# Kernel tuning notes

Measured on AMD Instinct MI355X. Metric: run time of the kernel, lower is better.

Reference implementation:

```python
import jax, jax.numpy as jnp
import numpy as np

N_NODES = 10000
N_EDGES = 160000
IN_C = 32
OUT_C = 32
FC = 32
DIM = 3
RADIUS = 1.0
LN_EPS = 1e-5


def _layernorm(x, g, b):
    mu = jnp.mean(x, axis=-1, keepdims=True)
    var = jnp.mean(jnp.square(x - mu), axis=-1, keepdims=True)
    return (x - mu) * jax.lax.rsqrt(var + LN_EPS) * g + b


def setup_inputs() -> dict:
    key = jax.random.key(0)
    ks = jax.random.split(key, 10)
    inp = {
        "features": jax.random.normal(ks[0], (N_NODES, IN_C), dtype=jnp.float32),
        "hood_coords": jax.random.normal(ks[1], (N_EDGES, DIM), dtype=jnp.float32),
        "source": jax.random.randint(ks[2], (N_EDGES,), 0, N_NODES, dtype=jnp.int32),
        "target": jax.random.randint(ks[3], (N_EDGES,), 0, N_NODES, dtype=jnp.int32),
        # neural field params: Linear(DIM,FC) -> LN -> ReLU -> Linear(FC,FC) -> LN -> ReLU -> Linear(FC, IN_C*OUT_C) -> Tanh
        "W0": jax.random.normal(ks[4], (DIM, FC), dtype=jnp.float32) * 0.3,
        "b0": jnp.zeros((FC,), dtype=jnp.float32),
        "g0": jnp.ones((FC,), dtype=jnp.float32),
        "beta0": jnp.zeros((FC,), dtype=jnp.float32),
        "W1": jax.random.normal(ks[5], (FC, FC), dtype=jnp.float32) * 0.15,
        "b1": jnp.zeros((FC,), dtype=jnp.float32),
        "g1": jnp.ones((FC,), dtype=jnp.float32),
        "beta1": jnp.zeros((FC,), dtype=jnp.float32),
        "W2": jax.random.normal(ks[6], (FC, IN_C * OUT_C), dtype=jnp.float32) * 0.15,
        "b2": jnp.zeros((IN_C * OUT_C,), dtype=jnp.float32),
    }
    return inp


def reference(features, hood_coords, source, target,
              W0, b0, g0, beta0, W1, b1, g1, beta1, W2, b2):
    m = features.shape[0]
    # neural field: per-edge weight matrix w [E, OUT_C, IN_C]
    x = hood_coords / RADIUS
    h = jax.nn.relu(_layernorm(x @ W0 + b0, g0, beta0))
    h = jax.nn.relu(_layernorm(h @ W1 + b1, g1, beta1))
    w = jnp.tanh(h @ W2 + b2).reshape(-1, OUT_C, IN_C)
    # gather + batched matvec: out[e,o] = sum_i f[e,i] * w[e,o,i]
    f = features[source]
    oc = jnp.einsum('ni,noi->no', f, w)
    # scatter_mean over target nodes
    sums = jax.ops.segment_sum(oc, target, num_segments=m)
    counts = jax.ops.segment_sum(jnp.ones((target.shape[0],), dtype=oc.dtype),
                                 target, num_segments=m)
    counts = jnp.maximum(counts, 1.0)
    return sums / counts[:, None]
```

## Files before the change

### kernel.cpp

```cpp
#include <hip/hip_runtime.h>

#define LN_EPS 1e-5f

typedef __attribute__((ext_vector_type(8)))  short short8;
typedef __attribute__((ext_vector_type(4)))  float floatx4;
typedef __attribute__((ext_vector_type(16))) float floatx16;

__device__ __forceinline__ unsigned short f2bf(float x) {
    unsigned u = __float_as_uint(x);
    u += 0x7FFFu + ((u >> 16) & 1u);
    return (unsigned short)(u >> 16);
}

__global__ __launch_bounds__(256) void k_edge_mlp(
    const float* __restrict__ coords,
    const int*   __restrict__ target,
    const float* __restrict__ W0, const float* __restrict__ b0,
    const float* __restrict__ g0, const float* __restrict__ be0,
    const float* __restrict__ W1, const float* __restrict__ b1,
    const float* __restrict__ g1, const float* __restrict__ be1,
    const float* __restrict__ W2, unsigned short* __restrict__ w2frag,
    unsigned short* __restrict__ hfrag, int* __restrict__ counts,
    int* __restrict__ rank, int E, int nEB)
{
    const int tid = threadIdx.x;

    if (blockIdx.x >= nEB) {
        const int idx = (blockIdx.x - nEB) * 256 + tid;
        if (idx < 4096) {
            const int l  = idx & 63;
            const int ot = idx >> 6;
            const int t  = ot & 1;
            const int o  = ot >> 1;
            const int row = l & 31;
            const int kb  = t*16 + (l >> 5)*8;
            short8 v;
            #pragma unroll
            for (int b = 0; b < 8; ++b)
                v[b] = (short)f2bf(W2[(size_t)(kb + b)*1024 + o*32 + row]);
            ((short8*)w2frag)[idx] = v;
        }
        return;
    }

    __shared__ float sW0[3*32], sW1T[32*36];
    __shared__ float sb0[32], sg0[32], sbe0[32], sb1[32], sg1[32], sbe1[32];
    for (int i = tid; i < 32*32; i += 256) {
        const int o = i & 31, c = i >> 5;
        sW1T[o*36 + c] = W1[i];
    }
    if (tid < 96) sW0[tid] = W0[tid];
    if (tid < 32) {
        sb0[tid] = b0[tid];  sg0[tid] = g0[tid];  sbe0[tid] = be0[tid];
        sb1[tid] = b1[tid];  sg1[tid] = g1[tid];  sbe1[tid] = be1[tid];
    }
    __syncthreads();

    const int e = blockIdx.x * 256 + tid;
    if (e >= E) return;

    const float x0 = coords[e*3+0];
    const float x1 = coords[e*3+1];
    const float x2 = coords[e*3+2];

    float h[32];
    #pragma unroll
    for (int o = 0; o < 32; ++o)
        h[o] = x0*sW0[o] + x1*sW0[32+o] + x2*sW0[64+o] + sb0[o];

    {
        float mu = 0.f;
        #pragma unroll
        for (int o = 0; o < 32; ++o) mu += h[o];
        mu *= (1.f/32.f);
        float var = 0.f;
        #pragma unroll
        for (int o = 0; o < 32; ++o) { float d = h[o]-mu; var += d*d; }
        var *= (1.f/32.f);
        const float inv = rsqrtf(var + LN_EPS);
        #pragma unroll
        for (int o = 0; o < 32; ++o)
            h[o] = fmaxf((h[o]-mu)*inv*sg0[o] + sbe0[o], 0.f);
    }

    float h2[32];
    #pragma unroll
    for (int o = 0; o < 32; ++o) {
        float s = sb1[o];
        #pragma unroll
        for (int c4 = 0; c4 < 8; ++c4) {
            const floatx4 wv = *reinterpret_cast<const floatx4*>(&sW1T[o*36 + c4*4]);
            s += h[c4*4+0]*wv[0] + h[c4*4+1]*wv[1]
               + h[c4*4+2]*wv[2] + h[c4*4+3]*wv[3];
        }
        h2[o] = s;
    }

    {
        float mu = 0.f;
        #pragma unroll
        for (int o = 0; o < 32; ++o) mu += h2[o];
        mu *= (1.f/32.f);
        float var = 0.f;
        #pragma unroll
        for (int o = 0; o < 32; ++o) { float d = h2[o]-mu; var += d*d; }
        var *= (1.f/32.f);
        const float inv = rsqrtf(var + LN_EPS);
        #pragma unroll
        for (int o = 0; o < 32; ++o)
            h2[o] = fmaxf((h2[o]-mu)*inv*sg1[o] + sbe1[o], 0.f);
    }

    const int et = e >> 5, er = e & 31;
    short8* base = (short8*)(hfrag) + (size_t)et * 128;
    #pragma unroll
    for (int t = 0; t < 2; ++t) {
        #pragma unroll
        for (int kg = 0; kg < 2; ++kg) {
            short8 v;
            #pragma unroll
            for (int b = 0; b < 8; ++b) v[b] = (short)f2bf(h2[t*16 + kg*8 + b]);
            base[t*64 + kg*32 + er] = v;
        }
    }

    rank[e] = atomicAdd(&counts[target[e]], 1);
}

__global__ __launch_bounds__(1024) void k_scan(
    const int* __restrict__ counts, int* __restrict__ offs, int N)
{
    __shared__ int wsum[16];
    const int t = threadIdx.x;
    const int lane = t & 63, w = t >> 6;
    const int CH = (N + 1023) >> 10;
    const int beg = t * CH;

    int s = 0;
    for (int k = 0; k < CH; ++k) {
        const int i = beg + k;
        if (i < N) s += counts[i];
    }
    int incl = s;
    #pragma unroll
    for (int d = 1; d < 64; d <<= 1) {
        const int x = __shfl_up(incl, d);
        if (lane >= d) incl += x;
    }
    if (lane == 63) wsum[w] = incl;
    __syncthreads();
    if (t == 0) {
        int run = 0;
        #pragma unroll
        for (int i = 0; i < 16; ++i) { const int v = wsum[i]; wsum[i] = run; run += v; }
    }
    __syncthreads();
    const int base = wsum[w] + incl - s;
    int run = base;
    for (int k = 0; k < CH; ++k) {
        const int i = beg + k;
        if (i < N) { offs[i] = run; run += counts[i]; }
    }
    if (t == 1023) offs[N] = base + s;
}

__global__ __launch_bounds__(256) void k_field_mfma(
    const unsigned short* __restrict__ hfrag,
    const unsigned short* __restrict__ w2frag,
    const float* __restrict__ features,
    const int*   __restrict__ src,
    const int*   __restrict__ tgt,
    const int*   __restrict__ rank,
    const int*   __restrict__ offs,
    const float* __restrict__ b2,
    unsigned short* __restrict__ ocP,
    int netiles)
{
    __shared__ float s_b2s[1024];
    __shared__ unsigned int sOC[2][32*9];
    __shared__ int sP[2][32];
    const int tid = threadIdx.x;
    const float KE = 2.8853900817779268f;
    #pragma unroll
    for (int r = 0; r < 4; ++r) s_b2s[tid + 256*r] = KE * b2[tid + 256*r];

    const int lane = tid & 63;
    const int wq   = tid >> 6;
    const int jh   = blockIdx.x & 1;
    const int W    = jh*4 + wq;
    const int h5   = lane >> 5;
    const int ecol = lane & 31;
    const float* b2base = &s_b2s[W*128 + 4*h5];
    const int str = tid >> 3;
    const int sti = tid & 7;

    short8 afr[8];
    #pragma unroll
    for (int u = 0; u < 8; ++u)
        afr[u] = ((const short8*)w2frag)[(W*8 + u)*64 + lane];
    __syncthreads();

    const floatx16 z16 = {0.f,0.f,0.f,0.f,0.f,0.f,0.f,0.f,
                          0.f,0.f,0.f,0.f,0.f,0.f,0.f,0.f};

    const int nunits = 2*netiles;
    int buf = 0;
    for (int unit = blockIdx.x; unit < nunits; unit += gridDim.x, buf ^= 1) {
        const int et = unit >> 1;
        const int e0 = et << 5;
        const short8 bs0 = ((const short8*)hfrag)[et*128 + lane];
        const short8 bs1 = ((const short8*)hfrag)[et*128 + 64 + lane];

        const int sN = src[e0 + ecol];
        if (tid < 32) sP[buf][ecol] = offs[tgt[e0 + ecol]] + rank[e0 + ecol];

        floatx4 fv[4];
        float fsl = 0.f;
        #pragma unroll
        for (int rq = 0; rq < 4; ++rq) {
            fv[rq] = *reinterpret_cast<const floatx4*>(
                         features + (size_t)sN*32 + rq*8 + 4*h5);
            #pragma unroll
            for (int rr = 0; rr < 4; ++rr) fsl += fv[rq][rr];
        }

        float q[4];
        #pragma unroll
        for (int u = 0; u < 4; ++u) {
            floatx16 d = __builtin_amdgcn_mfma_f32_32x32x16_bf16(afr[2*u],   bs0, z16, 0, 0, 0);
            d          = __builtin_amdgcn_mfma_f32_32x32x16_bf16(afr[2*u+1], bs1, d,   0, 0, 0);
            float sf0 = 0.f, sf1 = 0.f, sf2 = 0.f, sf3 = 0.f;
            #pragma unroll
            for (int qq = 0; qq < 4; ++qq) {
                const floatx4 bq = *reinterpret_cast<const floatx4*>(b2base + u*32 + 8*qq);
                const float t0 = fmaf(d[qq*4+0], KE, bq[0]);
                sf0 = fmaf(fv[qq][0], __builtin_amdgcn_rcpf(__builtin_amdgcn_exp2f(t0) + 1.0f), sf0);
                const float t1 = fmaf(d[qq*4+1], KE, bq[1]);
                sf1 = fmaf(fv[qq][1], __builtin_amdgcn_rcpf(__builtin_amdgcn_exp2f(t1) + 1.0f), sf1);
                const float t2 = fmaf(d[qq*4+2], KE, bq[2]);
                sf2 = fmaf(fv[qq][2], __builtin_amdgcn_rcpf(__builtin_amdgcn_exp2f(t2) + 1.0f), sf2);
                const float t3 = fmaf(d[qq*4+3], KE, bq[3]);
                sf3 = fmaf(fv[qq][3], __builtin_amdgcn_rcpf(__builtin_amdgcn_exp2f(t3) + 1.0f), sf3);
            }
            const float sf = (sf0 + sf1) + (sf2 + sf3);
            const float v  = fmaf(-2.0f, sf, fsl);
            q[u] = v + __shfl_xor(v, 32);
        }

        if (lane < 32) {
            const unsigned d0 = ((unsigned)f2bf(q[1]) << 16) | f2bf(q[0]);
            const unsigned d1 = ((unsigned)f2bf(q[3]) << 16) | f2bf(q[2]);
            sOC[buf][ecol*9 + wq*2]     = d0;
            sOC[buf][ecol*9 + wq*2 + 1] = d1;
        }
        __syncthreads();
        ((unsigned int*)ocP)[(size_t)sP[buf][str]*16 + jh*8 + sti] = sOC[buf][str*9 + sti];
    }
}

__global__ __launch_bounds__(256) void k_gather(
    const unsigned short* __restrict__ ocP,
    const int* __restrict__ offs,
    float* __restrict__ out, int N)
{
    const int node = blockIdx.x * 4 + (threadIdx.x >> 6);
    const int lane = threadIdx.x & 63;
    if (node >= N) return;
    const int r = lane >> 3;
    const int c = lane & 7;
    const int beg = offs[node], end = offs[node + 1];

    float a0 = 0.f, a1 = 0.f, a2 = 0.f, a3 = 0.f;
    for (int k = beg + r; k < end; k += 8) {
        const uint2 v = *reinterpret_cast<const uint2*>(ocP + (size_t)k*32 + c*4);
        a0 += __uint_as_float(v.x << 16);
        a1 += __uint_as_float(v.x & 0xFFFF0000u);
        a2 += __uint_as_float(v.y << 16);
        a3 += __uint_as_float(v.y & 0xFFFF0000u);
    }
    #pragma unroll
    for (int m = 8; m < 64; m <<= 1) {
        a0 += __shfl_xor(a0, m);
        a1 += __shfl_xor(a1, m);
        a2 += __shfl_xor(a2, m);
        a3 += __shfl_xor(a3, m);
    }
    if (lane < 8) {
        const float rinv = __builtin_amdgcn_rcpf(fmaxf((float)(end - beg), 1.0f));
        floatx4 o4 = {a0*rinv, a1*rinv, a2*rinv, a3*rinv};
        *reinterpret_cast<floatx4*>(out + (size_t)node*32 + lane*4) = o4;
    }
}

extern "C" void kernel_launch(void* const* d_in, const int* in_sizes, int n_in,
                              void* d_out, int out_size, void* d_ws, size_t ws_size,
                              hipStream_t stream)
{
    const float* features = (const float*)d_in[0];
    const float* coords   = (const float*)d_in[1];
    const int*   src      = (const int*)  d_in[2];
    const int*   tgt      = (const int*)  d_in[3];
    const float* W0  = (const float*)d_in[4];
    const float* b0  = (const float*)d_in[5];
    const float* g0  = (const float*)d_in[6];
    const float* be0 = (const float*)d_in[7];
    const float* W1  = (const float*)d_in[8];
    const float* b1  = (const float*)d_in[9];
    const float* g1  = (const float*)d_in[10];
    const float* be1 = (const float*)d_in[11];
    const float* W2  = (const float*)d_in[12];
    const float* b2  = (const float*)d_in[13];

    const int E = in_sizes[2];
    const int N = in_sizes[0] / 32;

    char* p = (char*)d_ws;
    unsigned short* hfrag  = (unsigned short*)p;  p += (size_t)E*32*2;
    unsigned short* ocP    = (unsigned short*)p;  p += (size_t)E*32*2;
    unsigned short* w2frag = (unsigned short*)p;  p += 32*1024*2;
    int* rankArr = (int*)p;  p += (size_t)E*4;
    int* counts  = (int*)p;  p += (size_t)N*4;
    int* offs    = (int*)p;  p += (size_t)(N+1)*4;

    (void)hipMemsetAsync(counts, 0, (size_t)N*4, stream);

    const int nEB = (E + 255)/256;
    k_edge_mlp<<<nEB + 16, 256, 0, stream>>>(
        coords, tgt, W0, b0, g0, be0, W1, b1, g1, be1, W2, w2frag,
        hfrag, counts, rankArr, E, nEB);

    k_scan<<<1, 1024, 0, stream>>>(counts, offs, N);

    const int netiles = E / 32;
    k_field_mfma<<<5000, 256, 0, stream>>>(
        hfrag, w2frag, features, src, tgt, rankArr, offs, b2, ocP, netiles);

    k_gather<<<(N + 3)/4, 256, 0, stream>>>(ocP, offs, (float*)d_out, N);
}
```

Baseline: 112.7 us.

## Fuse count scan into edge MLP via last-block pattern; retune field kernel grid

Removes the separate single-block scan launch by having the final block of the edge-MLP kernel, found with an atomic done counter and threadfence, perform the exclusive scan of counts from shared memory. It also adds a launch-bounds occupancy hint and shrinks the field kernel grid from 5000 to 2000 blocks, presumably relying on a grid-stride loop. The fused kernel now reserves 40KB of static shared memory per block, which can lower occupancy of the MLP phase, and the scan runs on 256 threads instead of 1024.

New measurement: 153.5 us. +36.1%, slower.

```diff
diff --git a/kernel.cpp b/kernel.cpp
--- a/kernel.cpp
+++ b/kernel.cpp
@@ -21,125 +21,133 @@
     const float* __restrict__ g1, const float* __restrict__ be1,
     const float* __restrict__ W2, unsigned short* __restrict__ w2frag,
     unsigned short* __restrict__ hfrag, int* __restrict__ counts,
-    int* __restrict__ rank, int E, int nEB)
+    int* __restrict__ rank, int* __restrict__ offs, int* __restrict__ done,
+    int E, int nEB, int nTotal, int N)
 {
+    __shared__ float sW0[3*32], sW1T[32*36];
+    __shared__ float sb0[32], sg0[32], sbe0[32], sb1[32], sg1[32], sbe1[32];
+    __shared__ int   sC2[10240];
+    __shared__ int   wsum2[4];
+    __shared__ int   sLast;
     const int tid = threadIdx.x;
 
     if (blockIdx.x >= nEB) {
         const int idx = (blockIdx.x - nEB) * 256 + tid;
-        if (idx < 4096) {
-            const int l  = idx & 63;
-            const int ot = idx >> 6;
-            const int t  = ot & 1;
-            const int o  = ot >> 1;
-            const int row = l & 31;
-            const int kb  = t*16 + (l >> 5)*8;
-            short8 v;
-            #pragma unroll
-            for (int b = 0; b < 8; ++b)
-                v[b] = (short)f2bf(W2[(size_t)(kb + b)*1024 + o*32 + row]);
-            ((short8*)w2frag)[idx] = v;
-        }
-        return;
-    }
-
-    __shared__ float sW0[3*32], sW1T[32*36];
-    __shared__ float sb0[32], sg0[32], sbe0[32], sb1[32], sg1[32], sbe1[32];
-    for (int i = tid; i < 32*32; i += 256) {
-        const int o = i & 31, c = i >> 5;
-        sW1T[o*36 + c] = W1[i];
-    }
-    if (tid < 96) sW0[tid] = W0[tid];
-    if (tid < 32) {
-        sb0[tid] = b0[tid];  sg0[tid] = g0[tid];  sbe0[tid] = be0[tid];
-        sb1[tid] = b1[tid];  sg1[tid] = g1[tid];  sbe1[tid] = be1[tid];
-    }
-    __syncthreads();
-
-    const int e = blockIdx.x * 256 + tid;
-    if (e >= E) return;
-
-    const float x0 = coords[e*3+0];
-    const float x1 = coords[e*3+1];
-    const float x2 = coords[e*3+2];
-
-    float h[32];
-    #pragma unroll
-    for (int o = 0; o < 32; ++o)
-        h[o] = x0*sW0[o] + x1*sW0[32+o] + x2*sW0[64+o] + sb0[o];
-
-    {
-        float mu = 0.f;
+        const int l  = idx & 63;
+        const int ot = idx >> 6;
+        const int t  = ot & 1;
+        const int o  = ot >> 1;
+        const int row = l & 31;
+        const int kb  = t*16 + (l >> 5)*8;
+        short8 v;
         #pragma unroll
-        for (int o = 0; o < 32; ++o) mu += h[o];
-        mu *= (1.f/32.f);
-        float var = 0.f;
-        #pragma unroll
-        for (int o = 0; o < 32; ++o) { float d = h[o]-mu; var += d*d; }
-        var *= (1.f/32.f);
-        const float inv = rsqrtf(var + LN_EPS);
-        #pragma unroll
-        for (int o = 0; o < 32; ++o)
-            h[o] = fmaxf((h[o]-mu)*inv*sg0[o] + sbe0[o], 0.f);
-    }
-
-    float h2[32];
-    #pragma unroll
-    for (int o = 0; o < 32; ++o) {
-        float s = sb1[o];
-        #pragma unroll
-        for (int c4 = 0; c4 < 8; ++c4) {
-            const floatx4 wv = *reinterpret_cast<const floatx4*>(&sW1T[o*36 + c4*4]);
-            s += h[c4*4+0]*wv[0] + h[c4*4+1]*wv[1]
-               + h[c4*4+2]*wv[2] + h[c4*4+3]*wv[3];
-        }
-        h2[o] = s;
-    }
-
-    {
-        float mu = 0.f;
-        #pragma unroll
-        for (int o = 0; o < 32; ++o) mu += h2[o];
-        mu *= (1.f/32.f);
-        float var = 0.f;
-        #pragma unroll
-        for (int o = 0; o < 32; ++o) { float d = h2[o]-mu; var += d*d; }
-        var *= (1.f/32.f);
-        const float inv = rsqrtf(var + LN_EPS);
-        #pragma unroll
-        for (int o = 0; o < 32; ++o)
-            h2[o] = fmaxf((h2[o]-mu)*inv*sg1[o] + sbe1[o], 0.f);
-    }
-
-    const int et = e >> 5, er = e & 31;
-    short8* base = (short8*)(hfrag) + (size_t)et * 128;
-    #pragma unroll
-    for (int t = 0; t < 2; ++t) {
-        #pragma unroll
-        for (int kg = 0; kg < 2; ++kg) {
-            short8 v;
-            #pragma unroll
-            for (int b = 0; b < 8; ++b) v[b] = (short)f2bf(h2[t*16 + kg*8 + b]);
-            base[t*64 + kg*32 + er] = v;
-        }
-    }
-
-    rank[e] = atomicAdd(&counts[target[e]], 1);
-}
-
-__global__ __launch_bounds__(1024) void k_scan(
-    const int* __restrict__ counts, int* __restrict__ offs, int N)
-{
-    __shared__ int wsum[16];
-    const int t = threadIdx.x;
-    const int lane = t & 63, w = t >> 6;
-    const int CH = (N + 1023) >> 10;
-    const int beg = t * CH;
-
+        for (int b = 0; b < 8; ++b)
+            v[b] = (short)f2bf(W2[(size_t)(kb + b)*1024 + o*32 + row]);
+        ((short8*)w2frag)[idx] = v;
+    } else {
+        for (int i = tid; i < 32*32; i += 256) {
+            const int o = i & 31, c = i >> 5;
+            sW1T[o*36 + c] = W1[i];
+        }
+        if (tid < 96) sW0[tid] = W0[tid];
+        if (tid < 32) {
+            sb0[tid] = b0[tid];  sg0[tid] = g0[tid];  sbe0[tid] = be0[tid];
+            sb1[tid] = b1[tid];  sg1[tid] = g1[tid];  sbe1[tid] = be1[tid];
+        }
+        __syncthreads();
+
+        const int e = blockIdx.x * 256 + tid;
+        if (e < E) {
+            const float x0 = coords[e*3+0];
+            const float x1 = coords[e*3+1];
+            const float x2 = coords[e*3+2];
+
+            float h[32];
+            #pragma unroll
+            for (int o = 0; o < 32; ++o)
+                h[o] = x0*sW0[o] + x1*sW0[32+o] + x2*sW0[64+o] + sb0[o];
+
+            {
+                float mu = 0.f;
+                #pragma unroll
+                for (int o = 0; o < 32; ++o) mu += h[o];
+                mu *= (1.f/32.f);
+                float var = 0.f;
+                #pragma unroll
+                for (int o = 0; o < 32; ++o) { float d = h[o]-mu; var += d*d; }
+                var *= (1.f/32.f);
+                const float inv = rsqrtf(var + LN_EPS);
+                #pragma unroll
+                for (int o = 0; o < 32; ++o)
+                    h[o] = fmaxf((h[o]-mu)*inv*sg0[o] + sbe0[o], 0.f);
+            }
+
+            float h2[32];
+            #pragma unroll
+            for (int o = 0; o < 32; ++o) {
+                float s = sb1[o];
+                #pragma unroll
+                for (int c4 = 0; c4 < 8; ++c4) {
+                    const floatx4 wv = *reinterpret_cast<const floatx4*>(&sW1T[o*36 + c4*4]);
+                    s += h[c4*4+0]*wv[0] + h[c4*4+1]*wv[1]
+                       + h[c4*4+2]*wv[2] + h[c4*4+3]*wv[3];
+                }
+                h2[o] = s;
+            }
+
+            {
+                float mu = 0.f;
+                #pragma unroll
+                for (int o = 0; o < 32; ++o) mu += h2[o];
+                mu *= (1.f/32.f);
+                float var = 0.f;
+                #pragma unroll
+                for (int o = 0; o < 32; ++o) { float d = h2[o]-mu; var += d*d; }
+                var *= (1.f/32.f);
+                const float inv = rsqrtf(var + LN_EPS);
+                #pragma unroll
+                for (int o = 0; o < 32; ++o)
+                    h2[o] = fmaxf((h2[o]-mu)*inv*sg1[o] + sbe1[o], 0.f);
+            }
+
+            const int et = e >> 5, er = e & 31;
+            short8* base = (short8*)(hfrag) + (size_t)et * 128;
+            #pragma unroll
+            for (int t = 0; t < 2; ++t) {
+                #pragma unroll
+                for (int kg = 0; kg < 2; ++kg) {
+                    short8 v;
+                    #pragma unroll
+                    for (int b = 0; b < 8; ++b) v[b] = (short)f2bf(h2[t*16 + kg*8 + b]);
+                    base[t*64 + kg*32 + er] = v;
+                }
+            }
+
+            rank[e] = atomicAdd(&counts[target[e]], 1);
+        }
+    }
+
+    __syncthreads();
+    __threadfence();
+    if (tid == 0) {
+        const int prev = atomicAdd(done, 1);
+        sLast = (prev == nTotal - 1) ? 1 : 0;
+    }
+    __syncthreads();
+    if (!sLast) return;
+
+    __threadfence();
+    const volatile int* vc = (const volatile int*)counts;
+    for (int i = tid; i < N; i += 256) sC2[i] = vc[i];
+    __syncthreads();
+
+    const int CH2 = (N + 255) >> 8;
+    const int lane = tid & 63, w = tid >> 6;
+    const int beg = tid * CH2;
     int s = 0;
-    for (int k = 0; k < CH; ++k) {
+    for (int k = 0; k < CH2; ++k) {
         const int i = beg + k;
-        if (i < N) s += counts[i];
+        if (i < N) s += sC2[i];
     }
     int incl = s;
     #pragma unroll
@@ -147,24 +155,26 @@
         const int x = __shfl_up(incl, d);
         if (lane >= d) incl += x;
     }
-    if (lane == 63) wsum[w] = incl;
-    __syncthreads();
-    if (t == 0) {
+    if (lane == 63) wsum2[w] = incl;
+    __syncthreads();
+    if (tid == 0) {
         int run = 0;
         #pragma unroll
-        for (int i = 0; i < 16; ++i) { const int v = wsum[i]; wsum[i] = run; run += v; }
-    }
-    __syncthreads();
-    const int base = wsum[w] + incl - s;
-    int run = base;
-    for (int k = 0; k < CH; ++k) {
+        for (int i = 0; i < 4; ++i) { const int v = wsum2[i]; wsum2[i] = run; run += v; }
+    }
+    __syncthreads();
+    const int base2 = wsum2[w] + incl - s;
+    int run = base2;
+    for (int k = 0; k < CH2; ++k) {
         const int i = beg + k;
-        if (i < N) { offs[i] = run; run += counts[i]; }
-    }
-    if (t == 1023) offs[N] = base + s;
-}
-
-__global__ __launch_bounds__(256) void k_field_mfma(
+        if (i < N) { const int c = sC2[i]; sC2[i] = run; run += c; }
+    }
+    __syncthreads();
+    for (int i = tid; i < N; i += 256) offs[i] = sC2[i];
+    if (tid == 255) offs[N] = base2 + s;
+}
+
+__global__ __launch_bounds__(256, 3) void k_field_mfma(
     const unsigned short* __restrict__ hfrag,
     const unsigned short* __restrict__ w2frag,
     const float* __restrict__ features,
@@ -320,19 +330,19 @@
     unsigned short* w2frag = (unsigned short*)p;  p += 32*1024*2;
     int* rankArr = (int*)p;  p += (size_t)E*4;
     int* counts  = (int*)p;  p += (size_t)N*4;
+    int* done    = (int*)p;  p += 4;
     int* offs    = (int*)p;  p += (size_t)(N+1)*4;
 
-    (void)hipMemsetAsync(counts, 0, (size_t)N*4, stream);
+    (void)hipMemsetAsync(counts, 0, ((size_t)N + 1) * 4, stream);
 
     const int nEB = (E + 255)/256;
-    k_edge_mlp<<<nEB + 16, 256, 0, stream>>>(
+    const int nTotal = nEB + 16;
+    k_edge_mlp<<<nTotal, 256, 0, stream>>>(
         coords, tgt, W0, b0, g0, be0, W1, b1, g1, be1, W2, w2frag,
-        hfrag, counts, rankArr, E, nEB);
-
-    k_scan<<<1, 1024, 0, stream>>>(counts, offs, N);
+        hfrag, counts, rankArr, offs, done, E, nEB, nTotal, N);
 
     const int netiles = E / 32;
-    k_field_mfma<<<5000, 256, 0, stream>>>(
+    k_field_mfma<<<2000, 256, 0, stream>>>(
         hfrag, w2frag, features, src, tgt, rankArr, offs, b2, ocP, netiles);
 
     k_gather<<<(N + 3)/4, 256, 0, stream>>>(ocP, offs, (float*)d_out, N);
```
